# Optimization experiments

Hardware: AMD Instinct MI355X
Metric: run time of the kernel (lower is better)

The kernel has to match this reference:

```python
import jax, jax.numpy as jnp
import numpy as np

TOP_K = 2


def setup_inputs() -> dict:
    key = jax.random.key(0)
    k0, k1, k2, k3 = jax.random.split(key, 4)
    T, H, E, I = 512, 2048, 16, 1024  # tokens, hidden, experts, intermediate
    return {
        "hidden_states": jax.random.normal(k0, (T, H), jnp.float32),
        "router_weight": jax.random.normal(k1, (E, H), jnp.float32) * 0.02,
        "w13": jax.random.normal(k2, (E, H, 2 * I), jnp.float32) * 0.02,  # fused gate+up
        "w2": jax.random.normal(k3, (E, I, H), jnp.float32) * 0.02,        # down proj
    }


def reference(hidden_states, router_weight, w13, w2):
    x = hidden_states                                   # [T, H]
    E = router_weight.shape[0]
    # Router: linear (no bias) -> softmax -> top-k -> renormalize
    logits = x @ router_weight.T                        # [T, E]
    probs = jax.nn.softmax(logits, axis=-1)
    vals, idx = jax.lax.top_k(probs, TOP_K)             # [T, K]
    vals = vals / jnp.sum(vals, axis=-1, keepdims=True)
    # Dense combine weights [T, E]: zero except the top-k experts per token
    cw = jnp.sum(jax.nn.one_hot(idx, E, dtype=x.dtype) * vals[..., None], axis=1)
    # Scan over experts; each expert runs a SwiGLU MLP over all tokens,
    # scaled by its (mostly-zero) combine weight. Keeps peak memory at [T, I].
    def body(acc, params):
        w13_e, w2_e, cw_e = params                      # [H,2I], [I,H], [T]
        g, u = jnp.split(x @ w13_e, 2, axis=-1)         # [T, I] each
        acc = acc + cw_e[:, None] * ((jax.nn.silu(g) * u) @ w2_e)
        return acc, None
    out, _ = jax.lax.scan(body, jnp.zeros_like(x), (w13, w2, cw.T))
    return out
```

## Files before the change

### kernel.cpp

```cpp
#include <hip/hip_runtime.h>

#define T_TOK 512
#define HID   2048
#define NEXP  16
#define IDIM  1024
#define KC    64

typedef __attribute__((ext_vector_type(8))) short bf16x8;
typedef __attribute__((ext_vector_type(4))) float f32x4;
typedef __attribute__((ext_vector_type(4))) float float4v;

__device__ __forceinline__ unsigned short f2bf(float f) {
    union { float f; unsigned u; } v; v.f = f;
    return (unsigned short)((v.u + 0x7FFFu + ((v.u >> 16) & 1u)) >> 16);
}

__device__ __forceinline__ bf16x8 pack8(const float* s) {
    bf16x8 r;
#pragma unroll
    for (int i = 0; i < 8; ++i) r[i] = (short)f2bf(s[i]);
    return r;
}

__global__ __launch_bounds__(256) void router_kernel(
    const float* __restrict__ x, const float* __restrict__ rw,
    int* __restrict__ cnt, int* __restrict__ tok,
    int* __restrict__ rowid, float* __restrict__ wt)
{
    int t = blockIdx.x;
    int tid = threadIdx.x;
    const float* xr = x + (size_t)t * HID;

    float acc[NEXP];
#pragma unroll
    for (int e = 0; e < NEXP; ++e) acc[e] = 0.f;

    for (int k = tid; k < HID; k += 256) {
        float xv = xr[k];
#pragma unroll
        for (int e = 0; e < NEXP; ++e) acc[e] += xv * rw[e * HID + k];
    }

    __shared__ float red[4][NEXP];
    int lane = tid & 63, wv = tid >> 6;
#pragma unroll
    for (int e = 0; e < NEXP; ++e) {
        float v = acc[e];
#pragma unroll
        for (int off = 32; off > 0; off >>= 1) v += __shfl_down(v, off);
        if (lane == 0) red[wv][e] = v;
    }
    __syncthreads();

    if (tid == 0) {
        float l[NEXP];
        float mx = -1e30f;
#pragma unroll
        for (int e = 0; e < NEXP; ++e) {
            l[e] = red[0][e] + red[1][e] + red[2][e] + red[3][e];
            mx = fmaxf(mx, l[e]);
        }
        float s = 0.f;
#pragma unroll
        for (int e = 0; e < NEXP; ++e) { l[e] = __expf(l[e] - mx); s += l[e]; }
        float inv_s = 1.f / s;
        int i0 = 0; float v0 = -1.f;
        int i1 = 0; float v1 = -2.f;
#pragma unroll
        for (int e = 0; e < NEXP; ++e) {
            float p = l[e] * inv_s;
            if (p > v0)      { v1 = v0; i1 = i0; v0 = p; i0 = e; }
            else if (p > v1) { v1 = p; i1 = e; }
        }
        float inv = 1.f / (v0 + v1);
        int p0 = atomicAdd(&cnt[i0], 1);
        tok[i0 * T_TOK + p0] = t; rowid[i0 * T_TOK + p0] = 2 * t;     wt[i0 * T_TOK + p0] = v0 * inv;
        int p1 = atomicAdd(&cnt[i1], 1);
        tok[i1 * T_TOK + p1] = t; rowid[i1 * T_TOK + p1] = 2 * t + 1; wt[i1 * T_TOK + p1] = v1 * inv;
    }
}

#define LOADW(buf, kk_, stride_) { _Pragma("unroll") \
    for (int j = 0; j < 8; ++j) \
        buf[j] = *(const float4v*)(wsrc + (size_t)((kk_) + kg * 8 + j) * (stride_)); }

#define CVTW(buf) { _Pragma("unroll") \
    for (int j2 = 0; j2 < 4; ++j2) { \
        float tmp[8]; \
        _Pragma("unroll") for (int j = 0; j < 8; ++j) tmp[j] = buf[j][j2]; \
        int col = c32 * 4 + j2; \
        *(bf16x8*)((char*)Ws + ((col * 128 + kg * 16) ^ ((col & 7) << 4))) = pack8(tmp); } }

#define LOADX(buf, kk_) { _Pragma("unroll") \
    for (int f = 0; f < 8; ++f) buf[f] = *(const float4v*)(xsrc + (kk_) + f * 4); }

#define CVTX(buf) { _Pragma("unroll") \
    for (int f = 0; f < 4; ++f) { \
        float tmp[8]; \
        _Pragma("unroll") for (int i = 0; i < 4; ++i) { tmp[i] = buf[2*f][i]; tmp[4+i] = buf[2*f+1][i]; } \
        *(bf16x8*)((char*)Xs + ((xrow * 128 + xq * 64 + f * 16) ^ xswz)) = pack8(tmp); } }

#define LOADH(buf, kk_) { _Pragma("unroll") \
    for (int j = 0; j < 4; ++j) \
        buf[j] = *(const float4v*)((const char*)hsrc + (size_t)(kk_) * 2 + j * 16); }

#define CVTH(buf) { _Pragma("unroll") \
    for (int j = 0; j < 4; ++j) \
        *(float4v*)((char*)Xs + ((xrow * 128 + xq * 64 + j * 16) ^ xswz)) = buf[j]; }

__global__ __launch_bounds__(512) void gemm1_kernel(
    const float* __restrict__ x, const float* __restrict__ w13,
    const int* __restrict__ cnt, const int* __restrict__ tok,
    const int* __restrict__ rowid, const float* __restrict__ wt,
    unsigned short* __restrict__ h)
{
    int bid = blockIdx.x;
    int e  = bid >> 4;
    int c0 = (bid & 15) * 64;
    int n = cnt[e];
    int tid = threadIdx.x;

    __shared__ short Xs[128 * KC];
    __shared__ short Ws[128 * KC];
    __shared__ int   tks[128];
    __shared__ int   rws[128];
    __shared__ float wts[128];

    const float* wbase = w13 + (size_t)e * HID * (2 * IDIM);

    bool isW = tid < 256;
    int rtid = isW ? tid : (tid - 256);
    int c32 = rtid & 31, kg = rtid >> 5;
    const float* wsrc = wbase + ((c32 < 16) ? (c0 + c32 * 4)
                                            : (IDIM + c0 + (c32 - 16) * 4));
    int xrow = rtid >> 1, xq = rtid & 1;
    int xswz = (xrow & 7) << 4;

    int wave = tid >> 6, lane = tid & 63;
    int wm = wave & 3, wn = wave >> 2;
    int lr = lane & 15, lh = lane >> 4;
    int swzA = (lr & 7) << 4;

    for (int t0 = 0; t0 < n; t0 += 128) {
        int nt = min(128, n - t0);
        __syncthreads();
        if (tid < 128) {
            int idx = t0 + min(tid, nt - 1);
            tks[tid] = tok[e * T_TOK + idx];
            rws[tid] = rowid[e * T_TOK + idx];
            wts[tid] = wt[e * T_TOK + idx];
        }
        __syncthreads();

        const float* xsrc = x + (size_t)tks[xrow] * HID + xq * 32;

        f32x4 accG[2][2], accU[2][2];
#pragma unroll
        for (int i = 0; i < 2; ++i)
#pragma unroll
            for (int j = 0; j < 2; ++j) { accG[i][j] = (f32x4)0.f; accU[i][j] = (f32x4)0.f; }

        float4v bufA[8], bufB[8];
        if (isW) { LOADW(bufA, 0, 2 * IDIM); } else { LOADX(bufA, 0); }

#define G1_MFMA() { _Pragma("unroll") \
        for (int s = 0; s < 2; ++s) { \
            _Pragma("unroll") for (int mf = 0; mf < 2; ++mf) { \
                if (wm * 32 + mf * 16 < nt) { \
                    int kb = (s * 32 + lh * 8) * 2; \
                    bf16x8 a = *(const bf16x8*)((char*)Xs + (((wm*32 + mf*16 + lr) * 128 + kb) ^ swzA)); \
                    _Pragma("unroll") for (int cf = 0; cf < 2; ++cf) { \
                        int colg = wn * 32 + cf * 16 + lr; \
                        bf16x8 bg = *(const bf16x8*)((char*)Ws + ((colg * 128 + kb) ^ swzA)); \
                        accG[mf][cf] = __builtin_amdgcn_mfma_f32_16x16x32_bf16(a, bg, accG[mf][cf], 0, 0, 0); \
                        bf16x8 bu = *(const bf16x8*)((char*)Ws + (((64 + colg) * 128 + kb) ^ swzA)); \
                        accU[mf][cf] = __builtin_amdgcn_mfma_f32_16x16x32_bf16(a, bu, accU[mf][cf], 0, 0, 0); \
                    } \
                } \
            } \
        } }

        for (int kk = 0; kk < HID; kk += 2 * KC) {
            if (isW) { LOADW(bufB, kk + KC, 2 * IDIM); CVTW(bufA); }
            else     { LOADX(bufB, kk + KC);           CVTX(bufA); }
            __syncthreads();
            G1_MFMA();
            __syncthreads();
            if (kk + 2 * KC < HID) {
                if (isW) { LOADW(bufA, kk + 2 * KC, 2 * IDIM); } else { LOADX(bufA, kk + 2 * KC); }
            }
            if (isW) { CVTW(bufB); } else { CVTX(bufB); }
            __syncthreads();
            G1_MFMA();
            __syncthreads();
        }

#pragma unroll
        for (int mf = 0; mf < 2; ++mf)
#pragma unroll
            for (int cf = 0; cf < 2; ++cf)
#pragma unroll
                for (int r = 0; r < 4; ++r) {
                    int row = wm * 32 + mf * 16 + lh * 4 + r;
                    if (row < nt) {
                        float g = accG[mf][cf][r], u = accU[mf][cf][r];
                        float sg = g / (1.f + __expf(-g));
                        float v = wts[row] * sg * u;
                        h[(size_t)rws[row] * IDIM + c0 + wn * 32 + cf * 16 + lr] = f2bf(v);
                    }
                }
    }
}

__global__ __launch_bounds__(512) void gemm2_kernel(
    const unsigned short* __restrict__ h, const float* __restrict__ w2,
    const int* __restrict__ cnt, const int* __restrict__ tok,
    const int* __restrict__ rowid,
    float* __restrict__ out)
{
    int bid = blockIdx.x;
    int e  = bid >> 4;
    int c0 = (bid & 15) * 128;
    int n = cnt[e];
    int tid = threadIdx.x;

    __shared__ short Xs[128 * KC];
    __shared__ short Ws[128 * KC];
    __shared__ int   tks[128];
    __shared__ int   rws[128];

    const float* wbase = w2 + (size_t)e * IDIM * HID;

    bool isW = tid < 256;
    int rtid = isW ? tid : (tid - 256);
    int c32 = rtid & 31, kg = rtid >> 5;
    const float* wsrc = wbase + c0 + c32 * 4;
    int xrow = rtid >> 1, xq = rtid & 1;
    int xswz = (xrow & 7) << 4;

    int wave = tid >> 6, lane = tid & 63;
    int wm = wave & 3, wn = wave >> 2;
    int lr = lane & 15, lh = lane >> 4;
    int swzA = (lr & 7) << 4;

    for (int t0 = 0; t0 < n; t0 += 128) {
        int nt = min(128, n - t0);
        __syncthreads();
        if (tid < 128) {
            int idx = t0 + min(tid, nt - 1);
            tks[tid] = tok[e * T_TOK + idx];
            rws[tid] = rowid[e * T_TOK + idx];
        }
        __syncthreads();

        const unsigned short* hsrc = h + (size_t)rws[xrow] * IDIM + xq * 32;

        f32x4 acc[2][4];
#pragma unroll
        for (int i = 0; i < 2; ++i)
#pragma unroll
            for (int j = 0; j < 4; ++j) acc[i][j] = (f32x4)0.f;

        float4v bufA[8], bufB[8];
        if (isW) { LOADW(bufA, 0, HID); } else { LOADH(bufA, 0); }

#define G2_MFMA() { _Pragma("unroll") \
        for (int s = 0; s < 2; ++s) { \
            _Pragma("unroll") for (int mf = 0; mf < 2; ++mf) { \
                if (wm * 32 + mf * 16 < nt) { \
                    int kb = (s * 32 + lh * 8) * 2; \
                    bf16x8 a = *(const bf16x8*)((char*)Xs + (((wm*32 + mf*16 + lr) * 128 + kb) ^ swzA)); \
                    _Pragma("unroll") for (int cf = 0; cf < 4; ++cf) { \
                        int col = wn * 64 + cf * 16 + lr; \
                        bf16x8 b = *(const bf16x8*)((char*)Ws + ((col * 128 + kb) ^ swzA)); \
                        acc[mf][cf] = __builtin_amdgcn_mfma_f32_16x16x32_bf16(a, b, acc[mf][cf], 0, 0, 0); \
                    } \
                } \
            } \
        } }

        for (int kk = 0; kk < IDIM; kk += 2 * KC) {
            if (isW) { LOADW(bufB, kk + KC, HID); CVTW(bufA); }
            else     { LOADH(bufB, kk + KC);      CVTH(bufA); }
            __syncthreads();
            G2_MFMA();
            __syncthreads();
            if (kk + 2 * KC < IDIM) {
                if (isW) { LOADW(bufA, kk + 2 * KC, HID); } else { LOADH(bufA, kk + 2 * KC); }
            }
            if (isW) { CVTW(bufB); } else { CVTH(bufB); }
            __syncthreads();
            G2_MFMA();
            __syncthreads();
        }

#pragma unroll
        for (int mf = 0; mf < 2; ++mf)
#pragma unroll
            for (int cf = 0; cf < 4; ++cf)
#pragma unroll
                for (int r = 0; r < 4; ++r) {
                    int row = wm * 32 + mf * 16 + lh * 4 + r;
                    if (row < nt)
                        atomicAdd(&out[(size_t)tks[row] * HID + c0 + wn * 64 + cf * 16 + lr],
                                  acc[mf][cf][r]);
                }
    }
}

extern "C" void kernel_launch(void* const* d_in, const int* in_sizes, int n_in,
                              void* d_out, int out_size, void* d_ws, size_t ws_size,
                              hipStream_t stream) {
    const float* x   = (const float*)d_in[0];
    const float* rw  = (const float*)d_in[1];
    const float* w13 = (const float*)d_in[2];
    const float* w2  = (const float*)d_in[3];
    float* out = (float*)d_out;

    int* cnt   = (int*)d_ws;
    int* tok   = cnt + 64;
    int* rowid = tok + NEXP * T_TOK;
    float* wt  = (float*)(rowid + NEXP * T_TOK);
    unsigned short* h = (unsigned short*)((char*)d_ws + 131072);

    hipMemsetAsync(out, 0, (size_t)T_TOK * HID * sizeof(float), stream);
    hipMemsetAsync(cnt, 0, 64 * sizeof(int), stream);

    router_kernel<<<T_TOK, 256, 0, stream>>>(x, rw, cnt, tok, rowid, wt);
    gemm1_kernel<<<256, 512, 0, stream>>>(x, w13, cnt, tok, rowid, wt, h);
    gemm2_kernel<<<256, 512, 0, stream>>>(h, w2, cnt, tok, rowid, out);
}
```

Before: 142.5 us.

## Pre-convert activations to bf16 in router and halve GEMM column tiles

The router kernel now also writes a bf16 copy of the hidden states, so gemm1 loads bf16 activations directly instead of converting fp32 tokens again in every column block. Both expert GEMMs halve the column tile width and double the grid to 512 blocks. All 512 threads now cooperate on both weight and activation staging rather than splitting into loader roles, and each wave owns one 16-row slice. The aim is more parallelism across CUs and less redundant conversion work, at the cost of reading the activation tile more times per weight byte and adding an extra workspace buffer.

```diff
diff --git a/kernel.cpp b/kernel.cpp
--- a/kernel.cpp
+++ b/kernel.cpp
@@ -15,6 +15,10 @@
     return (unsigned short)((v.u + 0x7FFFu + ((v.u >> 16) & 1u)) >> 16);
 }
 
+__device__ __forceinline__ unsigned pack2(float lo, float hi) {
+    return (unsigned)f2bf(lo) | ((unsigned)f2bf(hi) << 16);
+}
+
 __device__ __forceinline__ bf16x8 pack8(const float* s) {
     bf16x8 r;
 #pragma unroll
@@ -25,11 +29,22 @@
 __global__ __launch_bounds__(256) void router_kernel(
     const float* __restrict__ x, const float* __restrict__ rw,
     int* __restrict__ cnt, int* __restrict__ tok,
-    int* __restrict__ rowid, float* __restrict__ wt)
+    int* __restrict__ rowid, float* __restrict__ wt,
+    unsigned short* __restrict__ xb)
 {
     int t = blockIdx.x;
     int tid = threadIdx.x;
     const float* xr = x + (size_t)t * HID;
+
+    {
+        int c = tid * 8;
+        float4v a = *(const float4v*)(xr + c);
+        float4v b = *(const float4v*)(xr + c + 4);
+        float tmp[8];
+#pragma unroll
+        for (int i = 0; i < 4; ++i) { tmp[i] = a[i]; tmp[4 + i] = b[i]; }
+        *(bf16x8*)(xb + (size_t)t * HID + c) = pack8(tmp);
+    }
 
     float acc[NEXP];
 #pragma unroll
@@ -80,64 +95,51 @@
     }
 }
 
-#define LOADW(buf, kk_, stride_) { _Pragma("unroll") \
-    for (int j = 0; j < 8; ++j) \
-        buf[j] = *(const float4v*)(wsrc + (size_t)((kk_) + kg * 8 + j) * (stride_)); }
-
-#define CVTW(buf) { _Pragma("unroll") \
+#define LOADW(buf, kk_, stride_) { \
+    buf[0] = *(const float4v*)(wsrc + (size_t)((kk_) + kg * 2)     * (stride_)); \
+    buf[1] = *(const float4v*)(wsrc + (size_t)((kk_) + kg * 2 + 1) * (stride_)); }
+
+#define STOREW(buf) { _Pragma("unroll") \
     for (int j2 = 0; j2 < 4; ++j2) { \
-        float tmp[8]; \
-        _Pragma("unroll") for (int j = 0; j < 8; ++j) tmp[j] = buf[j][j2]; \
-        int col = c32 * 4 + j2; \
-        *(bf16x8*)((char*)Ws + ((col * 128 + kg * 16) ^ ((col & 7) << 4))) = pack8(tmp); } }
-
-#define LOADX(buf, kk_) { _Pragma("unroll") \
-    for (int f = 0; f < 8; ++f) buf[f] = *(const float4v*)(xsrc + (kk_) + f * 4); }
-
-#define CVTX(buf) { _Pragma("unroll") \
-    for (int f = 0; f < 4; ++f) { \
-        float tmp[8]; \
-        _Pragma("unroll") for (int i = 0; i < 4; ++i) { tmp[i] = buf[2*f][i]; tmp[4+i] = buf[2*f+1][i]; } \
-        *(bf16x8*)((char*)Xs + ((xrow * 128 + xq * 64 + f * 16) ^ xswz)) = pack8(tmp); } }
-
-#define LOADH(buf, kk_) { _Pragma("unroll") \
-    for (int j = 0; j < 4; ++j) \
-        buf[j] = *(const float4v*)((const char*)hsrc + (size_t)(kk_) * 2 + j * 16); }
-
-#define CVTH(buf) { _Pragma("unroll") \
-    for (int j = 0; j < 4; ++j) \
-        *(float4v*)((char*)Xs + ((xrow * 128 + xq * 64 + j * 16) ^ xswz)) = buf[j]; }
-
-__global__ __launch_bounds__(512) void gemm1_kernel(
-    const float* __restrict__ x, const float* __restrict__ w13,
+        int colw = cg * 4 + j2; \
+        *(unsigned*)((char*)Ws + ((colw * 128 + kg * 4) ^ ((colw & 7) << 4))) = \
+            pack2(buf[0][j2], buf[1][j2]); } }
+
+#define LOADX(buf, kk_) { \
+    buf[0] = *(const bf16x8*)(xsrc + (kk_)); \
+    buf[1] = *(const bf16x8*)(xsrc + (kk_) + 8); }
+
+#define STOREX(buf) { \
+    *(bf16x8*)((char*)Xs + ((xrow * 128 + xq * 32)      ^ xswz)) = buf[0]; \
+    *(bf16x8*)((char*)Xs + ((xrow * 128 + xq * 32 + 16) ^ xswz)) = buf[1]; }
+
+__global__ __launch_bounds__(512, 4) void gemm1_kernel(
+    const unsigned short* __restrict__ xb, const float* __restrict__ w13,
     const int* __restrict__ cnt, const int* __restrict__ tok,
     const int* __restrict__ rowid, const float* __restrict__ wt,
     unsigned short* __restrict__ h)
 {
     int bid = blockIdx.x;
-    int e  = bid >> 4;
-    int c0 = (bid & 15) * 64;
+    int e  = bid >> 5;
+    int c0 = (bid & 31) * 32;
     int n = cnt[e];
     int tid = threadIdx.x;
 
-    __shared__ short Xs[128 * KC];
-    __shared__ short Ws[128 * KC];
+    __shared__ __align__(16) short Xs[128 * KC];
+    __shared__ __align__(16) short Ws[64 * KC];
     __shared__ int   tks[128];
     __shared__ int   rws[128];
     __shared__ float wts[128];
 
     const float* wbase = w13 + (size_t)e * HID * (2 * IDIM);
 
-    bool isW = tid < 256;
-    int rtid = isW ? tid : (tid - 256);
-    int c32 = rtid & 31, kg = rtid >> 5;
-    const float* wsrc = wbase + ((c32 < 16) ? (c0 + c32 * 4)
-                                            : (IDIM + c0 + (c32 - 16) * 4));
-    int xrow = rtid >> 1, xq = rtid & 1;
+    int cg = tid & 15, kg = tid >> 4;
+    const float* wsrc = wbase + ((cg < 8) ? (c0 + cg * 4)
+                                          : (IDIM + c0 + (cg - 8) * 4));
+    int xrow = tid >> 2, xq = tid & 3;
     int xswz = (xrow & 7) << 4;
 
     int wave = tid >> 6, lane = tid & 63;
-    int wm = wave & 3, wn = wave >> 2;
     int lr = lane & 15, lh = lane >> 4;
     int swzA = (lr & 7) << 4;
 
@@ -152,94 +154,84 @@
         }
         __syncthreads();
 
-        const float* xsrc = x + (size_t)tks[xrow] * HID + xq * 32;
-
-        f32x4 accG[2][2], accU[2][2];
-#pragma unroll
-        for (int i = 0; i < 2; ++i)
-#pragma unroll
-            for (int j = 0; j < 2; ++j) { accG[i][j] = (f32x4)0.f; accU[i][j] = (f32x4)0.f; }
-
-        float4v bufA[8], bufB[8];
-        if (isW) { LOADW(bufA, 0, 2 * IDIM); } else { LOADX(bufA, 0); }
-
-#define G1_MFMA() { _Pragma("unroll") \
-        for (int s = 0; s < 2; ++s) { \
-            _Pragma("unroll") for (int mf = 0; mf < 2; ++mf) { \
-                if (wm * 32 + mf * 16 < nt) { \
-                    int kb = (s * 32 + lh * 8) * 2; \
-                    bf16x8 a = *(const bf16x8*)((char*)Xs + (((wm*32 + mf*16 + lr) * 128 + kb) ^ swzA)); \
-                    _Pragma("unroll") for (int cf = 0; cf < 2; ++cf) { \
-                        int colg = wn * 32 + cf * 16 + lr; \
-                        bf16x8 bg = *(const bf16x8*)((char*)Ws + ((colg * 128 + kb) ^ swzA)); \
-                        accG[mf][cf] = __builtin_amdgcn_mfma_f32_16x16x32_bf16(a, bg, accG[mf][cf], 0, 0, 0); \
-                        bf16x8 bu = *(const bf16x8*)((char*)Ws + (((64 + colg) * 128 + kb) ^ swzA)); \
-                        accU[mf][cf] = __builtin_amdgcn_mfma_f32_16x16x32_bf16(a, bu, accU[mf][cf], 0, 0, 0); \
-                    } \
+        const unsigned short* xsrc = xb + (size_t)tks[xrow] * HID + xq * 16;
+
+        f32x4 accG[2], accU[2];
+#pragma unroll
+        for (int i = 0; i < 2; ++i) { accG[i] = (f32x4)0.f; accU[i] = (f32x4)0.f; }
+
+        float4v wbufA[2], wbufB[2];
+        bf16x8 xbufA[2], xbufB[2];
+        LOADW(wbufA, 0, 2 * IDIM); LOADX(xbufA, 0);
+
+#define G1_MFMA() { \
+        if (wave * 16 < nt) { _Pragma("unroll") \
+            for (int s = 0; s < 2; ++s) { \
+                int kb = (s * 32 + lh * 8) * 2; \
+                bf16x8 a = *(const bf16x8*)((char*)Xs + (((wave * 16 + lr) * 128 + kb) ^ swzA)); \
+                _Pragma("unroll") for (int cf = 0; cf < 2; ++cf) { \
+                    int colg = cf * 16 + lr; \
+                    bf16x8 bg = *(const bf16x8*)((char*)Ws + ((colg * 128 + kb) ^ swzA)); \
+                    accG[cf] = __builtin_amdgcn_mfma_f32_16x16x32_bf16(a, bg, accG[cf], 0, 0, 0); \
+                    bf16x8 bu = *(const bf16x8*)((char*)Ws + (((32 + colg) * 128 + kb) ^ swzA)); \
+                    accU[cf] = __builtin_amdgcn_mfma_f32_16x16x32_bf16(a, bu, accU[cf], 0, 0, 0); \
                 } \
             } \
         } }
 
         for (int kk = 0; kk < HID; kk += 2 * KC) {
-            if (isW) { LOADW(bufB, kk + KC, 2 * IDIM); CVTW(bufA); }
-            else     { LOADX(bufB, kk + KC);           CVTX(bufA); }
+            LOADW(wbufB, kk + KC, 2 * IDIM); LOADX(xbufB, kk + KC);
+            STOREW(wbufA); STOREX(xbufA);
             __syncthreads();
             G1_MFMA();
             __syncthreads();
-            if (kk + 2 * KC < HID) {
-                if (isW) { LOADW(bufA, kk + 2 * KC, 2 * IDIM); } else { LOADX(bufA, kk + 2 * KC); }
+            if (kk + 2 * KC < HID) { LOADW(wbufA, kk + 2 * KC, 2 * IDIM); LOADX(xbufA, kk + 2 * KC); }
+            STOREW(wbufB); STOREX(xbufB);
+            __syncthreads();
+            G1_MFMA();
+            __syncthreads();
+        }
+
+#pragma unroll
+        for (int cf = 0; cf < 2; ++cf)
+#pragma unroll
+            for (int r = 0; r < 4; ++r) {
+                int row = wave * 16 + lh * 4 + r;
+                if (row < nt) {
+                    float g = accG[cf][r], u = accU[cf][r];
+                    float sg = g / (1.f + __expf(-g));
+                    float v = wts[row] * sg * u;
+                    h[(size_t)rws[row] * IDIM + c0 + cf * 16 + lr] = f2bf(v);
+                }
             }
-            if (isW) { CVTW(bufB); } else { CVTX(bufB); }
-            __syncthreads();
-            G1_MFMA();
-            __syncthreads();
-        }
-
-#pragma unroll
-        for (int mf = 0; mf < 2; ++mf)
-#pragma unroll
-            for (int cf = 0; cf < 2; ++cf)
-#pragma unroll
-                for (int r = 0; r < 4; ++r) {
-                    int row = wm * 32 + mf * 16 + lh * 4 + r;
-                    if (row < nt) {
-                        float g = accG[mf][cf][r], u = accU[mf][cf][r];
-                        float sg = g / (1.f + __expf(-g));
-                        float v = wts[row] * sg * u;
-                        h[(size_t)rws[row] * IDIM + c0 + wn * 32 + cf * 16 + lr] = f2bf(v);
-                    }
-                }
-    }
-}
-
-__global__ __launch_bounds__(512) void gemm2_kernel(
+    }
+}
+
+__global__ __launch_bounds__(512, 4) void gemm2_kernel(
     const unsigned short* __restrict__ h, const float* __restrict__ w2,
     const int* __restrict__ cnt, const int* __restrict__ tok,
     const int* __restrict__ rowid,
     float* __restrict__ out)
 {
     int bid = blockIdx.x;
-    int e  = bid >> 4;
-    int c0 = (bid & 15) * 128;
+    int e  = bid >> 5;
+    int c0 = (bid & 31) * 64;
     int n = cnt[e];
     int tid = threadIdx.x;
 
-    __shared__ short Xs[128 * KC];
-    __shared__ short Ws[128 * KC];
+    __shared__ __align__(16) short Xs[128 * KC];
+    __shared__ __align__(16) short Ws[64 * KC];
     __shared__ int   tks[128];
     __shared__ int   rws[128];
 
     const float* wbase = w2 + (size_t)e * IDIM * HID;
 
-    bool isW = tid < 256;
-    int rtid = isW ? tid : (tid - 256);
-    int c32 = rtid & 31, kg = rtid >> 5;
-    const float* wsrc = wbase + c0 + c32 * 4;
-    int xrow = rtid >> 1, xq = rtid & 1;
+    int cg = tid & 15, kg = tid >> 4;
+    const float* wsrc = wbase + c0 + cg * 4;
+    int xrow = tid >> 2, xq = tid & 3;
     int xswz = (xrow & 7) << 4;
 
     int wave = tid >> 6, lane = tid & 63;
-    int wm = wave & 3, wn = wave >> 2;
     int lr = lane & 15, lh = lane >> 4;
     int swzA = (lr & 7) << 4;
 
@@ -253,58 +245,50 @@
         }
         __syncthreads();
 
-        const unsigned short* hsrc = h + (size_t)rws[xrow] * IDIM + xq * 32;
-
-        f32x4 acc[2][4];
-#pragma unroll
-        for (int i = 0; i < 2; ++i)
-#pragma unroll
-            for (int j = 0; j < 4; ++j) acc[i][j] = (f32x4)0.f;
-
-        float4v bufA[8], bufB[8];
-        if (isW) { LOADW(bufA, 0, HID); } else { LOADH(bufA, 0); }
-
-#define G2_MFMA() { _Pragma("unroll") \
-        for (int s = 0; s < 2; ++s) { \
-            _Pragma("unroll") for (int mf = 0; mf < 2; ++mf) { \
-                if (wm * 32 + mf * 16 < nt) { \
-                    int kb = (s * 32 + lh * 8) * 2; \
-                    bf16x8 a = *(const bf16x8*)((char*)Xs + (((wm*32 + mf*16 + lr) * 128 + kb) ^ swzA)); \
-                    _Pragma("unroll") for (int cf = 0; cf < 4; ++cf) { \
-                        int col = wn * 64 + cf * 16 + lr; \
-                        bf16x8 b = *(const bf16x8*)((char*)Ws + ((col * 128 + kb) ^ swzA)); \
-                        acc[mf][cf] = __builtin_amdgcn_mfma_f32_16x16x32_bf16(a, b, acc[mf][cf], 0, 0, 0); \
-                    } \
+        const unsigned short* xsrc = h + (size_t)rws[xrow] * IDIM + xq * 16;
+
+        f32x4 acc[4];
+#pragma unroll
+        for (int i = 0; i < 4; ++i) acc[i] = (f32x4)0.f;
+
+        float4v wbufA[2], wbufB[2];
+        bf16x8 xbufA[2], xbufB[2];
+        LOADW(wbufA, 0, HID); LOADX(xbufA, 0);
+
+#define G2_MFMA() { \
+        if (wave * 16 < nt) { _Pragma("unroll") \
+            for (int s = 0; s < 2; ++s) { \
+                int kb = (s * 32 + lh * 8) * 2; \
+                bf16x8 a = *(const bf16x8*)((char*)Xs + (((wave * 16 + lr) * 128 + kb) ^ swzA)); \
+                _Pragma("unroll") for (int cf = 0; cf < 4; ++cf) { \
+                    int col = cf * 16 + lr; \
+                    bf16x8 b = *(const bf16x8*)((char*)Ws + ((col * 128 + kb) ^ swzA)); \
+                    acc[cf] = __builtin_amdgcn_mfma_f32_16x16x32_bf16(a, b, acc[cf], 0, 0, 0); \
                 } \
             } \
         } }
 
         for (int kk = 0; kk < IDIM; kk += 2 * KC) {
-            if (isW) { LOADW(bufB, kk + KC, HID); CVTW(bufA); }
-            else     { LOADH(bufB, kk + KC);      CVTH(bufA); }
+            LOADW(wbufB, kk + KC, HID); LOADX(xbufB, kk + KC);
+            STOREW(wbufA); STOREX(xbufA);
             __syncthreads();
             G2_MFMA();
             __syncthreads();
-            if (kk + 2 * KC < IDIM) {
-                if (isW) { LOADW(bufA, kk + 2 * KC, HID); } else { LOADH(bufA, kk + 2 * KC); }
+            if (kk + 2 * KC < IDIM) { LOADW(wbufA, kk + 2 * KC, HID); LOADX(xbufA, kk + 2 * KC); }
+            STOREW(wbufB); STOREX(xbufB);
+            __syncthreads();
+            G2_MFMA();
+            __syncthreads();
+        }
+
+#pragma unroll
+        for (int cf = 0; cf < 4; ++cf)
+#pragma unroll
+            for (int r = 0; r < 4; ++r) {
+                int row = wave * 16 + lh * 4 + r;
+                if (row < nt)
+                    atomicAdd(&out[(size_t)tks[row] * HID + c0 + cf * 16 + lr], acc[cf][r]);
             }
-            if (isW) { CVTW(bufB); } else { CVTH(bufB); }
-            __syncthreads();
-            G2_MFMA();
-            __syncthreads();
-        }
-
-#pragma unroll
-        for (int mf = 0; mf < 2; ++mf)
-#pragma unroll
-            for (int cf = 0; cf < 4; ++cf)
-#pragma unroll
-                for (int r = 0; r < 4; ++r) {
-                    int row = wm * 32 + mf * 16 + lh * 4 + r;
-                    if (row < nt)
-                        atomicAdd(&out[(size_t)tks[row] * HID + c0 + wn * 64 + cf * 16 + lr],
-                                  acc[mf][cf][r]);
-                }
     }
 }
 
@@ -321,12 +305,13 @@
     int* tok   = cnt + 64;
     int* rowid = tok + NEXP * T_TOK;
     float* wt  = (float*)(rowid + NEXP * T_TOK);
-    unsigned short* h = (unsigned short*)((char*)d_ws + 131072);
+    unsigned short* h  = (unsigned short*)((char*)d_ws + 131072);
+    unsigned short* xb = (unsigned short*)((char*)d_ws + 131072 + 2097152);
 
     hipMemsetAsync(out, 0, (size_t)T_TOK * HID * sizeof(float), stream);
     hipMemsetAsync(cnt, 0, 64 * sizeof(int), stream);
 
-    router_kernel<<<T_TOK, 256, 0, stream>>>(x, rw, cnt, tok, rowid, wt);
-    gemm1_kernel<<<256, 512, 0, stream>>>(x, w13, cnt, tok, rowid, wt, h);
-    gemm2_kernel<<<256, 512, 0, stream>>>(h, w2, cnt, tok, rowid, out);
-}
+    router_kernel<<<T_TOK, 256, 0, stream>>>(x, rw, cnt, tok, rowid, wt, xb);
+    gemm1_kernel<<<512, 512, 0, stream>>>(xb, w13, cnt, tok, rowid, wt, h);
+    gemm2_kernel<<<512, 512, 0, stream>>>(h, w2, cnt, tok, rowid, out);
+}
```

Measured after the change: 133.2 us. -6.5%, faster.
